# Optimization experiments

Measured on AMD Instinct MI355X. Metric: run time of the kernel, lower is better.

Reference implementation:

```python
import jax, jax.numpy as jnp
import numpy as np

NUM_AGENTS = 256
STATE_DIM = 12 * NUM_AGENTS
CONTROL_DIM = 4 * NUM_AGENTS
MASS = 0.5
HIDDEN = 100
BATCH = 8192


def lambertw(x):
    # Principal branch for x >= 0 via Halley iterations (jit/vjp friendly).
    w = jnp.log1p(x)
    for _ in range(30):
        ew = jnp.exp(w)
        f = w * ew - x
        denom = ew * (w + 1.0) - (w + 2.0) * f / (2.0 * (w + 1.0))
        w = w - f / denom
    return w


def setup_inputs() -> dict:
    key = jax.random.key(0)
    ks = jax.random.split(key, 8)
    scale1 = 1.0 / np.sqrt(STATE_DIM + 1)
    scale2 = 1.0 / np.sqrt(HIDDEN)
    return {
        "z": jax.random.normal(ks[0], (BATCH, STATE_DIM), dtype=jnp.float32),
        "t": jax.random.uniform(ks[1], (BATCH, 1), dtype=jnp.float32),
        "W1": jax.random.normal(ks[2], (STATE_DIM + 1, HIDDEN), dtype=jnp.float32) * scale1,
        "b1": jnp.zeros((HIDDEN,), dtype=jnp.float32),
        "W2": jax.random.normal(ks[3], (HIDDEN, HIDDEN), dtype=jnp.float32) * scale2,
        "b2": jnp.zeros((HIDDEN,), dtype=jnp.float32),
        "W3": jax.random.normal(ks[4], (HIDDEN, STATE_DIM), dtype=jnp.float32) * scale2,
        "b3": jnp.zeros((STATE_DIM,), dtype=jnp.float32),
    }


def reference(z, t, W1, b1, W2, b2, W3, b3):
    # p_net: MLP on (t, z) producing cost parameters p (B, STATE_DIM)
    x = jnp.concatenate([t, z], axis=-1)
    h = jnp.tanh(x @ W1 + b1)
    h = jnp.tanh(h @ W2 + b2)
    p = h @ W3 + b3

    B = p.shape[0]
    pr = p.reshape(B, NUM_AGENTS, 12)
    # Linear cost vector c over controls: agent components (x,y,z adjoints)/m, psi, theta, phi.
    c = jnp.stack(
        [(pr[..., 6] + pr[..., 7] + pr[..., 8]) / MASS, pr[..., 9], pr[..., 10], pr[..., 11]],
        axis=-1,
    ).reshape(B, CONTROL_DIM)

    # Closed-form solution of min_u c^T u + exp(alpha * ||u||^2), alpha = 0.5/N:
    # u* = -k c with 2*alpha*k*exp(alpha*k^2*s) = 1, s = ||c||^2
    # => k = sqrt(W(s/(2*alpha)) / (2*alpha*s))
    alpha = 0.5 / NUM_AGENTS
    s = jnp.sum(c * c, axis=-1)  # (B,)
    w = lambertw(s / (2.0 * alpha))
    safe_s = jnp.where(s > 0, s, 1.0)
    k = jnp.sqrt(w / (2.0 * alpha * safe_s))
    k = jnp.where(s > 0, k, 0.0)
    ustar = -k[:, None] * c  # (B, CONTROL_DIM)
    return ustar
```

## Files before the change

### kernel.cpp

```cpp
#include <hip/hip_runtime.h>

#define DEV __device__ __forceinline__

typedef __bf16 bf16x8 __attribute__((ext_vector_type(8)));
typedef float f32x4 __attribute__((ext_vector_type(4)));
typedef short s16x8 __attribute__((ext_vector_type(8)));
typedef unsigned short u16x4 __attribute__((ext_vector_type(4)));

constexpr int B_ = 8192;
constexpr int S_ = 3072;
constexpr int H_ = 100;
constexpr int NP_ = 128;
constexpr int C_ = 1024;
constexpr int KS_ = 64;
constexpr int NIT_ = S_ / KS_;

constexpr size_t OFF_W1b = 0;
constexpr size_t OFF_W2b = OFF_W1b + (size_t)NP_ * S_ * 2;
constexpr size_t OFF_W3c = OFF_W2b + (size_t)NP_ * NP_ * 2;
constexpr size_t OFF_b3c = OFF_W3c + (size_t)C_ * NP_ * 2;
constexpr size_t OFF_h2b = OFF_b3c + (size_t)C_ * 4;

DEV unsigned short f2bf(float f) {
  union { float f; unsigned u; } x; x.f = f;
  return (unsigned short)((x.u + 0x7FFFu + ((x.u >> 16) & 1u)) >> 16);
}

DEV float lambertw0(float x) {
  float w = log1pf(x);
#pragma unroll
  for (int i = 0; i < 10; ++i) {
    float ew = expf(w);
    float f = fmaf(w, ew, -x);
    float wp1 = w + 1.0f;
    float den = ew * wp1 - (w + 2.0f) * f / (2.0f * wp1);
    w = w - f / den;
  }
  return w;
}

__global__ void k0_prep(const float* __restrict__ W1, const float* __restrict__ W2,
                        const float* __restrict__ W3, const float* __restrict__ b3,
                        unsigned char* __restrict__ ws) {
  int idx = blockIdx.x * 256 + threadIdx.x;
  constexpr int R1 = NP_ * S_;
  constexpr int R2 = R1 + NP_ * NP_;
  constexpr int R3 = R2 + C_ * NP_;
  constexpr int R4 = R3 + C_;
  if (idx < R1) {
    int n = idx / S_, k = idx - n * S_;
    float v = (n < H_) ? W1[(size_t)(k + 1) * H_ + n] : 0.0f;
    ((unsigned short*)(ws + OFF_W1b))[idx] = f2bf(v);
  } else if (idx < R2) {
    int j = idx - R1;
    int n = j >> 7, k = j & 127;
    float v = (n < H_ && k < H_) ? W2[(size_t)k * H_ + n] : 0.0f;
    ((unsigned short*)(ws + OFF_W2b))[j] = f2bf(v);
  } else if (idx < R3) {
    int j = idx - R2;
    int n = j >> 7, k = j & 127;
    float v = 0.0f;
    if (k < H_) {
      int a = n >> 2, cmp = n & 3;
      const float* row = W3 + (size_t)k * S_ + a * 12;
      v = (cmp == 0) ? 2.0f * (row[6] + row[7] + row[8]) : row[8 + cmp];
    }
    ((unsigned short*)(ws + OFF_W3c))[j] = f2bf(v);
  } else if (idx < R4) {
    int n = idx - R3;
    int a = n >> 2, cmp = n & 3;
    const float* row = b3 + a * 12;
    float v = (cmp == 0) ? 2.0f * (row[6] + row[7] + row[8]) : row[8 + cmp];
    ((float*)(ws + OFF_b3c))[n] = v;
  }
}

__global__ __launch_bounds__(512, 2) void k1_mlp(
    const float* __restrict__ z, const float* __restrict__ t,
    const float* __restrict__ W1, const float* __restrict__ b1,
    const float* __restrict__ b2, const unsigned char* __restrict__ wsr,
    unsigned short* __restrict__ h2b) {
  __shared__ __align__(16) unsigned char lds[40 * 1024 + 128];
  unsigned char* ldsA = lds;
  unsigned char* ldsB = lds + 8192;
  float* t_lds = (float*)(lds + 40 * 1024);

  const int tid = threadIdx.x;
  const int lane = tid & 63;
  const int w = tid >> 6;
  const int m = w & 1;
  const int q = w >> 1;
  const int rowbase = blockIdx.x * 32;

  const unsigned short* W1b = (const unsigned short*)(wsr + OFF_W1b);
  const unsigned short* W2b = (const unsigned short*)(wsr + OFF_W2b);

  if (tid < 32) t_lds[tid] = t[rowbase + tid];

  float b1c[2], w1tc[2], b2c[2];
#pragma unroll
  for (int e = 0; e < 2; ++e) {
    int col = (q * 2 + e) * 16 + (lane & 15);
    bool ok = col < H_;
    b1c[e] = ok ? b1[col] : 0.0f;
    w1tc[e] = ok ? W1[col] : 0.0f;
    b2c[e] = ok ? b2[col] : 0.0f;
  }

  const int zrow = tid >> 4;
  const int zk4 = (tid & 15) * 4;
  const int r0 = m * 16 + (lane & 15);
  const int kb0 = (lane >> 4) * 16;

  f32x4 acc[2];
  acc[0] = f32x4{0.f, 0.f, 0.f, 0.f};
  acc[1] = f32x4{0.f, 0.f, 0.f, 0.f};

  {
    float4 zv = *(const float4*)(z + (size_t)(rowbase + zrow) * S_ + zk4);
    u16x4 av; av[0] = f2bf(zv.x); av[1] = f2bf(zv.y); av[2] = f2bf(zv.z); av[3] = f2bf(zv.w);
    *(u16x4*)(ldsA + ((zrow * 128 + zk4 * 2) ^ ((zrow & 7) << 4))) = av;
#pragma unroll
    for (int s = 0; s < 2; ++s) {
      int p = s * 512 + tid;
      int n = p >> 3, k16 = p & 7;
      s16x8 v = *(const s16x8*)(W1b + (size_t)n * S_ + k16 * 8);
      *(s16x8*)(ldsB + ((n * 128 + k16 * 16) ^ ((n & 7) << 4))) = v;
    }
  }
  __syncthreads();

  for (int it = 0; it < NIT_; ++it) {
    const int cur = it & 1;
    unsigned char* Ac = ldsA + cur * 4096;
    unsigned char* Bc = ldsB + cur * 16384;
    const bool more = (it + 1 < NIT_);
    float4 zv;
    s16x8 bv0, bv1;
    if (more) {
      int kb = (it + 1) * KS_;
      zv = *(const float4*)(z + (size_t)(rowbase + zrow) * S_ + kb + zk4);
      {
        int p = tid;          int n = p >> 3, k16 = p & 7;
        bv0 = *(const s16x8*)(W1b + (size_t)n * S_ + kb + k16 * 8);
      }
      {
        int p = 512 + tid;    int n = p >> 3, k16 = p & 7;
        bv1 = *(const s16x8*)(W1b + (size_t)n * S_ + kb + k16 * 8);
      }
    }
    bf16x8 a0 = *(const bf16x8*)(Ac + ((r0 * 128 + 0 + kb0) ^ ((r0 & 7) << 4)));
    bf16x8 a1 = *(const bf16x8*)(Ac + ((r0 * 128 + 64 + kb0) ^ ((r0 & 7) << 4)));
#pragma unroll
    for (int e = 0; e < 2; ++e) {
      int n = (q * 2 + e) * 16 + (lane & 15);
      bf16x8 bb0 = *(const bf16x8*)(Bc + ((n * 128 + 0 + kb0) ^ ((n & 7) << 4)));
      bf16x8 bb1 = *(const bf16x8*)(Bc + ((n * 128 + 64 + kb0) ^ ((n & 7) << 4)));
      acc[e] = __builtin_amdgcn_mfma_f32_16x16x32_bf16(a0, bb0, acc[e], 0, 0, 0);
      acc[e] = __builtin_amdgcn_mfma_f32_16x16x32_bf16(a1, bb1, acc[e], 0, 0, 0);
    }
    if (more) {
      unsigned char* An = ldsA + (cur ^ 1) * 4096;
      unsigned char* Bn = ldsB + (cur ^ 1) * 16384;
      u16x4 av; av[0] = f2bf(zv.x); av[1] = f2bf(zv.y); av[2] = f2bf(zv.z); av[3] = f2bf(zv.w);
      *(u16x4*)(An + ((zrow * 128 + zk4 * 2) ^ ((zrow & 7) << 4))) = av;
      {
        int p = tid;          int n = p >> 3, k16 = p & 7;
        *(s16x8*)(Bn + ((n * 128 + k16 * 16) ^ ((n & 7) << 4))) = bv0;
      }
      {
        int p = 512 + tid;    int n = p >> 3, k16 = p & 7;
        *(s16x8*)(Bn + ((n * 128 + k16 * 16) ^ ((n & 7) << 4))) = bv1;
      }
    }
    __syncthreads();
  }

#pragma unroll
  for (int e = 0; e < 2; ++e) {
    int col = (q * 2 + e) * 16 + (lane & 15);
#pragma unroll
    for (int i = 0; i < 4; ++i) {
      int r = m * 16 + ((lane >> 4) << 2) + i;
      float pre = acc[e][i] + b1c[e] + t_lds[r] * w1tc[e];
      *(unsigned short*)(ldsA + ((r * 256 + col * 2) ^ ((r & 7) << 4))) = f2bf(tanhf(pre));
    }
  }
#pragma unroll
  for (int s = 0; s < 4; ++s) {
    int p = s * 512 + tid;
    int n = p >> 4, k16 = p & 15;
    s16x8 v = *(const s16x8*)(W2b + n * 128 + k16 * 8);
    *(s16x8*)(ldsB + ((n * 256 + k16 * 16) ^ ((n & 7) << 4))) = v;
  }
  __syncthreads();

  f32x4 acc2[2];
  acc2[0] = f32x4{0.f, 0.f, 0.f, 0.f};
  acc2[1] = f32x4{0.f, 0.f, 0.f, 0.f};
#pragma unroll
  for (int ks = 0; ks < 4; ++ks) {
    bf16x8 a = *(const bf16x8*)(ldsA + ((r0 * 256 + ks * 64 + kb0) ^ ((r0 & 7) << 4)));
#pragma unroll
    for (int e = 0; e < 2; ++e) {
      int n = (q * 2 + e) * 16 + (lane & 15);
      bf16x8 b = *(const bf16x8*)(ldsB + ((n * 256 + ks * 64 + kb0) ^ ((n & 7) << 4)));
      acc2[e] = __builtin_amdgcn_mfma_f32_16x16x32_bf16(a, b, acc2[e], 0, 0, 0);
    }
  }
#pragma unroll
  for (int e = 0; e < 2; ++e) {
    int col = (q * 2 + e) * 16 + (lane & 15);
#pragma unroll
    for (int i = 0; i < 4; ++i) {
      int r = m * 16 + ((lane >> 4) << 2) + i;
      float h = tanhf(acc2[e][i] + b2c[e]);
      h2b[(size_t)(rowbase + r) * NP_ + col] = f2bf(h);
    }
  }
}

__global__ __launch_bounds__(512, 2) void k2_head(
    const unsigned char* __restrict__ wsr, float* __restrict__ uo) {
  __shared__ __align__(16) unsigned char ldsA[8192];
  __shared__ __align__(16) unsigned char ldsB[2][32768];
  __shared__ float s_part[32][4];
  __shared__ float k_lds[32];

  const int tid = threadIdx.x;
  const int lane = tid & 63;
  const int w = tid >> 6;
  const int m = w & 1;
  const int q = w >> 1;
  const int rowbase = blockIdx.x * 32;

  const unsigned short* h2b = (const unsigned short*)(wsr + OFF_h2b);
  const unsigned short* W3cb = (const unsigned short*)(wsr + OFF_W3c);
  const float* b3c = (const float*)(wsr + OFF_b3c);

  {
    int n = tid >> 4, k16 = tid & 15;
    s16x8 v = *(const s16x8*)(h2b + (size_t)(rowbase + n) * NP_ + k16 * 8);
    *(s16x8*)(ldsA + ((n * 256 + k16 * 16) ^ ((n & 7) << 4))) = v;
  }
#pragma unroll
  for (int s = 0; s < 4; ++s) {
    int p = s * 512 + tid;
    int n = p >> 4, k16 = p & 15;
    s16x8 v = *(const s16x8*)(W3cb + (size_t)n * NP_ + k16 * 8);
    *(s16x8*)(ldsB[0] + ((n * 256 + k16 * 16) ^ ((n & 7) << 4))) = v;
  }
  if (tid < 128) s_part[tid >> 2][tid & 3] = 0.0f;
  __syncthreads();

  const int r0 = m * 16 + (lane & 15);
  const int kb0 = (lane >> 4) * 16;
  bf16x8 af[4];
#pragma unroll
  for (int ks = 0; ks < 4; ++ks)
    af[ks] = *(const bf16x8*)(ldsA + ((r0 * 256 + ks * 64 + kb0) ^ ((r0 & 7) << 4)));

  f32x4 fr[16];
#pragma unroll
  for (int i = 0; i < 16; ++i) fr[i] = f32x4{0.f, 0.f, 0.f, 0.f};

#pragma unroll 8
  for (int ch = 0; ch < 8; ++ch) {
    const int cur = ch & 1;
    const bool more = ch < 7;
    s16x8 st0, st1, st2, st3;
    if (more) {
      int base = (ch + 1) * 128;
      { int p = tid;            int n = p >> 4, k16 = p & 15; st0 = *(const s16x8*)(W3cb + (size_t)(base + n) * NP_ + k16 * 8); }
      { int p = 512 + tid;      int n = p >> 4, k16 = p & 15; st1 = *(const s16x8*)(W3cb + (size_t)(base + n) * NP_ + k16 * 8); }
      { int p = 1024 + tid;     int n = p >> 4, k16 = p & 15; st2 = *(const s16x8*)(W3cb + (size_t)(base + n) * NP_ + k16 * 8); }
      { int p = 1536 + tid;     int n = p >> 4, k16 = p & 15; st3 = *(const s16x8*)(W3cb + (size_t)(base + n) * NP_ + k16 * 8); }
    }
#pragma unroll
    for (int e = 0; e < 2; ++e) {
      int nloc = (q + 4 * e) * 16 + (lane & 15);
#pragma unroll
      for (int ks = 0; ks < 4; ++ks) {
        bf16x8 b = *(const bf16x8*)(ldsB[cur] + ((nloc * 256 + ks * 64 + kb0) ^ ((nloc & 7) << 4)));
        fr[ch * 2 + e] = __builtin_amdgcn_mfma_f32_16x16x32_bf16(af[ks], b, fr[ch * 2 + e], 0, 0, 0);
      }
    }
    if (more) {
      unsigned char* Bn = ldsB[cur ^ 1];
      { int p = tid;        int n = p >> 4, k16 = p & 15; *(s16x8*)(Bn + ((n * 256 + k16 * 16) ^ ((n & 7) << 4))) = st0; }
      { int p = 512 + tid;  int n = p >> 4, k16 = p & 15; *(s16x8*)(Bn + ((n * 256 + k16 * 16) ^ ((n & 7) << 4))) = st1; }
      { int p = 1024 + tid; int n = p >> 4, k16 = p & 15; *(s16x8*)(Bn + ((n * 256 + k16 * 16) ^ ((n & 7) << 4))) = st2; }
      { int p = 1536 + tid; int n = p >> 4, k16 = p & 15; *(s16x8*)(Bn + ((n * 256 + k16 * 16) ^ ((n & 7) << 4))) = st3; }
    }
    __syncthreads();
  }

#pragma unroll
  for (int fi = 0; fi < 16; ++fi) {
    int ch = fi >> 1, e = fi & 1;
    int col = (ch * 8 + q + 4 * e) * 16 + (lane & 15);
    float bc = b3c[col];
    fr[fi][0] += bc; fr[fi][1] += bc; fr[fi][2] += bc; fr[fi][3] += bc;
  }
#pragma unroll
  for (int i = 0; i < 4; ++i) {
    float v = 0.f;
#pragma unroll
    for (int fi = 0; fi < 16; ++fi) v += fr[fi][i] * fr[fi][i];
    v += __shfl_xor(v, 1);
    v += __shfl_xor(v, 2);
    v += __shfl_xor(v, 4);
    v += __shfl_xor(v, 8);
    if ((lane & 15) == 0) s_part[m * 16 + ((lane >> 4) << 2) + i][q] = v;
  }
  __syncthreads();
  if (tid < 32) {
    float s = s_part[tid][0] + s_part[tid][1] + s_part[tid][2] + s_part[tid][3];
    float kk = 0.0f;
    if (s > 0.0f) {
      float wv = lambertw0(s * 256.0f);
      kk = sqrtf(wv * 256.0f / s);
    }
    k_lds[tid] = kk;
  }
  __syncthreads();
#pragma unroll
  for (int fi = 0; fi < 16; ++fi) {
    int ch = fi >> 1, e = fi & 1;
    int col = (ch * 8 + q + 4 * e) * 16 + (lane & 15);
#pragma unroll
    for (int i = 0; i < 4; ++i) {
      int r = m * 16 + ((lane >> 4) << 2) + i;
      uo[(size_t)(rowbase + r) * C_ + col] = -k_lds[r] * fr[fi][i];
    }
  }
}

extern "C" void kernel_launch(void* const* d_in, const int* in_sizes, int n_in,
                              void* d_out, int out_size, void* d_ws, size_t ws_size,
                              hipStream_t stream) {
  const float* z  = (const float*)d_in[0];
  const float* t  = (const float*)d_in[1];
  const float* W1 = (const float*)d_in[2];
  const float* b1 = (const float*)d_in[3];
  const float* W2 = (const float*)d_in[4];
  const float* b2 = (const float*)d_in[5];
  const float* W3 = (const float*)d_in[6];
  const float* b3 = (const float*)d_in[7];
  float* out = (float*)d_out;
  unsigned char* ws = (unsigned char*)d_ws;

  constexpr int PREP_ELEMS = NP_ * S_ + NP_ * NP_ + C_ * NP_ + C_;
  k0_prep<<<(PREP_ELEMS + 255) / 256, 256, 0, stream>>>(W1, W2, W3, b3, ws);
  k1_mlp<<<B_ / 32, 512, 0, stream>>>(z, t, W1, b1, b2, ws,
                                      (unsigned short*)(ws + OFF_h2b));
  k2_head<<<B_ / 32, 512, 0, stream>>>(ws, out);
}
```

Before: 59.10 us.

## Split first GEMM over K into four blocks with partial-sum reduction kernel

The first layer GEMM (B×3072 by 3072×128) is split along K into four independent blocks per row tile, each writing fp32 partial sums into the output buffer used as scratch. A new kernel sums the partials, applies bias, time term and tanh, then runs layer two. Block size drops to 256 threads with four waves each covering 64 columns. This raises grid parallelism from 256 to 1024 blocks to fill the GPU's compute units better, at the cost of an extra 16 MB partial write/read and an added kernel launch.

```diff
diff --git a/kernel.cpp b/kernel.cpp
--- a/kernel.cpp
+++ b/kernel.cpp
@@ -6,6 +6,7 @@
 typedef float f32x4 __attribute__((ext_vector_type(4)));
 typedef short s16x8 __attribute__((ext_vector_type(8)));
 typedef unsigned short u16x4 __attribute__((ext_vector_type(4)));
+typedef unsigned short u16x8 __attribute__((ext_vector_type(8)));
 
 constexpr int B_ = 8192;
 constexpr int S_ = 3072;
@@ -13,7 +14,9 @@
 constexpr int NP_ = 128;
 constexpr int C_ = 1024;
 constexpr int KS_ = 64;
-constexpr int NIT_ = S_ / KS_;
+constexpr int NSPLIT_ = 4;
+constexpr int KSP_ = S_ / NSPLIT_;
+constexpr int NIT_ = KSP_ / KS_;
 
 constexpr size_t OFF_W1b = 0;
 constexpr size_t OFF_W2b = OFF_W1b + (size_t)NP_ * S_ * 2;
@@ -75,15 +78,120 @@
   }
 }
 
-__global__ __launch_bounds__(512, 2) void k1_mlp(
-    const float* __restrict__ z, const float* __restrict__ t,
+__global__ __launch_bounds__(256, 4) void k1_gemm1(
+    const float* __restrict__ z, const unsigned char* __restrict__ wsr,
+    float* __restrict__ part) {
+  __shared__ __align__(16) unsigned char lds[40 * 1024];
+  unsigned char* ldsA = lds;
+  unsigned char* ldsB = lds + 8192;
+
+  const int tid = threadIdx.x;
+  const int lane = tid & 63;
+  const int w = tid >> 6;
+  const int m = w & 1;
+  const int q = w >> 1;
+  const int bid = blockIdx.x;
+  const int rt = bid >> 2;
+  const int h = bid & 3;
+  const int rowbase = rt * 32;
+  const int k0 = h * KSP_;
+
+  const unsigned short* W1b = (const unsigned short*)(wsr + OFF_W1b);
+
+  const int zrow = tid >> 3;
+  const int zk8 = (tid & 7) * 8;
+  const float* zp = z + (size_t)(rowbase + zrow) * S_ + k0 + zk8;
+  const int bn = tid >> 3;
+  const int bk16 = (tid & 7) * 8;
+  const unsigned short* bp = W1b + (size_t)bn * S_ + k0 + bk16;
+
+  const int aswz = ((zrow & 7) << 4);
+  const int abyte = zrow * 128 + zk8 * 2;
+  const int bswz = ((bn & 7) << 4);
+  const int bbyte0 = bn * 128 + bk16 * 2;
+
+  const int r0 = m * 16 + (lane & 15);
+  const int kb0 = (lane >> 4) * 16;
+
+  f32x4 acc[4];
+#pragma unroll
+  for (int e = 0; e < 4; ++e) acc[e] = f32x4{0.f, 0.f, 0.f, 0.f};
+
+  {
+    float4 za = *(const float4*)(zp);
+    float4 zb = *(const float4*)(zp + 4);
+    u16x8 av;
+    av[0] = f2bf(za.x); av[1] = f2bf(za.y); av[2] = f2bf(za.z); av[3] = f2bf(za.w);
+    av[4] = f2bf(zb.x); av[5] = f2bf(zb.y); av[6] = f2bf(zb.z); av[7] = f2bf(zb.w);
+    *(u16x8*)(ldsA + (abyte ^ aswz)) = av;
+#pragma unroll
+    for (int s = 0; s < 4; ++s) {
+      s16x8 v = *(const s16x8*)(bp + (size_t)(s * 32) * S_);
+      *(s16x8*)(ldsB + ((bbyte0 + s * 32 * 128) ^ bswz)) = v;
+    }
+  }
+  __syncthreads();
+
+  for (int it = 0; it < NIT_; ++it) {
+    const int cur = it & 1;
+    unsigned char* Ac = ldsA + cur * 4096;
+    unsigned char* Bc = ldsB + cur * 16384;
+    const bool more = (it + 1 < NIT_);
+    float4 za, zb;
+    s16x8 bv0, bv1, bv2, bv3;
+    if (more) {
+      const int ko = (it + 1) * KS_;
+      za = *(const float4*)(zp + ko);
+      zb = *(const float4*)(zp + ko + 4);
+      bv0 = *(const s16x8*)(bp + ko);
+      bv1 = *(const s16x8*)(bp + ko + (size_t)32 * S_);
+      bv2 = *(const s16x8*)(bp + ko + (size_t)64 * S_);
+      bv3 = *(const s16x8*)(bp + ko + (size_t)96 * S_);
+    }
+    bf16x8 a0 = *(const bf16x8*)(Ac + ((r0 * 128 + 0 + kb0) ^ ((r0 & 7) << 4)));
+    bf16x8 a1 = *(const bf16x8*)(Ac + ((r0 * 128 + 64 + kb0) ^ ((r0 & 7) << 4)));
+#pragma unroll
+    for (int e = 0; e < 4; ++e) {
+      int n = q * 64 + e * 16 + (lane & 15);
+      bf16x8 bb0 = *(const bf16x8*)(Bc + ((n * 128 + 0 + kb0) ^ ((n & 7) << 4)));
+      bf16x8 bb1 = *(const bf16x8*)(Bc + ((n * 128 + 64 + kb0) ^ ((n & 7) << 4)));
+      acc[e] = __builtin_amdgcn_mfma_f32_16x16x32_bf16(a0, bb0, acc[e], 0, 0, 0);
+      acc[e] = __builtin_amdgcn_mfma_f32_16x16x32_bf16(a1, bb1, acc[e], 0, 0, 0);
+    }
+    if (more) {
+      unsigned char* An = ldsA + (cur ^ 1) * 4096;
+      unsigned char* Bn = ldsB + (cur ^ 1) * 16384;
+      u16x8 av;
+      av[0] = f2bf(za.x); av[1] = f2bf(za.y); av[2] = f2bf(za.z); av[3] = f2bf(za.w);
+      av[4] = f2bf(zb.x); av[5] = f2bf(zb.y); av[6] = f2bf(zb.z); av[7] = f2bf(zb.w);
+      *(u16x8*)(An + (abyte ^ aswz)) = av;
+      *(s16x8*)(Bn + ((bbyte0 + 0 * 32 * 128) ^ bswz)) = bv0;
+      *(s16x8*)(Bn + ((bbyte0 + 1 * 32 * 128) ^ bswz)) = bv1;
+      *(s16x8*)(Bn + ((bbyte0 + 2 * 32 * 128) ^ bswz)) = bv2;
+      *(s16x8*)(Bn + ((bbyte0 + 3 * 32 * 128) ^ bswz)) = bv3;
+    }
+    __syncthreads();
+  }
+
+  float* pout = part + (size_t)h * B_ * NP_;
+#pragma unroll
+  for (int e = 0; e < 4; ++e) {
+    int col = q * 64 + e * 16 + (lane & 15);
+#pragma unroll
+    for (int i = 0; i < 4; ++i) {
+      int r = m * 16 + ((lane >> 4) << 2) + i;
+      pout[(size_t)(rowbase + r) * NP_ + col] = acc[e][i];
+    }
+  }
+}
+
+__global__ __launch_bounds__(256, 4) void k2a_mlp(
+    const float* __restrict__ part, const float* __restrict__ t,
     const float* __restrict__ W1, const float* __restrict__ b1,
     const float* __restrict__ b2, const unsigned char* __restrict__ wsr,
     unsigned short* __restrict__ h2b) {
-  __shared__ __align__(16) unsigned char lds[40 * 1024 + 128];
-  unsigned char* ldsA = lds;
-  unsigned char* ldsB = lds + 8192;
-  float* t_lds = (float*)(lds + 40 * 1024);
+  __shared__ __align__(16) unsigned char ldsA[8192];
+  __shared__ __align__(16) unsigned char ldsB[32768];
 
   const int tid = threadIdx.x;
   const int lane = tid & 63;
@@ -92,130 +200,70 @@
   const int q = w >> 1;
   const int rowbase = blockIdx.x * 32;
 
-  const unsigned short* W1b = (const unsigned short*)(wsr + OFF_W1b);
   const unsigned short* W2b = (const unsigned short*)(wsr + OFF_W2b);
 
-  if (tid < 32) t_lds[tid] = t[rowbase + tid];
-
-  float b1c[2], w1tc[2], b2c[2];
-#pragma unroll
-  for (int e = 0; e < 2; ++e) {
-    int col = (q * 2 + e) * 16 + (lane & 15);
-    bool ok = col < H_;
-    b1c[e] = ok ? b1[col] : 0.0f;
-    w1tc[e] = ok ? W1[col] : 0.0f;
-    b2c[e] = ok ? b2[col] : 0.0f;
-  }
-
-  const int zrow = tid >> 4;
-  const int zk4 = (tid & 15) * 4;
-  const int r0 = m * 16 + (lane & 15);
-  const int kb0 = (lane >> 4) * 16;
-
-  f32x4 acc[2];
-  acc[0] = f32x4{0.f, 0.f, 0.f, 0.f};
-  acc[1] = f32x4{0.f, 0.f, 0.f, 0.f};
-
   {
-    float4 zv = *(const float4*)(z + (size_t)(rowbase + zrow) * S_ + zk4);
-    u16x4 av; av[0] = f2bf(zv.x); av[1] = f2bf(zv.y); av[2] = f2bf(zv.z); av[3] = f2bf(zv.w);
-    *(u16x4*)(ldsA + ((zrow * 128 + zk4 * 2) ^ ((zrow & 7) << 4))) = av;
-#pragma unroll
-    for (int s = 0; s < 2; ++s) {
-      int p = s * 512 + tid;
-      int n = p >> 3, k16 = p & 7;
-      s16x8 v = *(const s16x8*)(W1b + (size_t)n * S_ + k16 * 8);
-      *(s16x8*)(ldsB + ((n * 128 + k16 * 16) ^ ((n & 7) << 4))) = v;
-    }
-  }
-  __syncthreads();
-
-  for (int it = 0; it < NIT_; ++it) {
-    const int cur = it & 1;
-    unsigned char* Ac = ldsA + cur * 4096;
-    unsigned char* Bc = ldsB + cur * 16384;
-    const bool more = (it + 1 < NIT_);
-    float4 zv;
-    s16x8 bv0, bv1;
-    if (more) {
-      int kb = (it + 1) * KS_;
-      zv = *(const float4*)(z + (size_t)(rowbase + zrow) * S_ + kb + zk4);
-      {
-        int p = tid;          int n = p >> 3, k16 = p & 7;
-        bv0 = *(const s16x8*)(W1b + (size_t)n * S_ + kb + k16 * 8);
+    const int row = tid >> 3;
+    const int col0 = (tid & 7) * 16;
+    const float* p0 = part + (size_t)(rowbase + row) * NP_ + col0;
+    f32x4 v[4];
+#pragma unroll
+    for (int p = 0; p < 4; ++p) {
+      v[p] = *(const f32x4*)(p0 + p * 4);
+#pragma unroll
+      for (int hh = 1; hh < NSPLIT_; ++hh) {
+        f32x4 u = *(const f32x4*)(p0 + (size_t)hh * B_ * NP_ + p * 4);
+        v[p][0] += u[0]; v[p][1] += u[1]; v[p][2] += u[2]; v[p][3] += u[3];
       }
-      {
-        int p = 512 + tid;    int n = p >> 3, k16 = p & 7;
-        bv1 = *(const s16x8*)(W1b + (size_t)n * S_ + kb + k16 * 8);
-      }
-    }
-    bf16x8 a0 = *(const bf16x8*)(Ac + ((r0 * 128 + 0 + kb0) ^ ((r0 & 7) << 4)));
-    bf16x8 a1 = *(const bf16x8*)(Ac + ((r0 * 128 + 64 + kb0) ^ ((r0 & 7) << 4)));
-#pragma unroll
-    for (int e = 0; e < 2; ++e) {
-      int n = (q * 2 + e) * 16 + (lane & 15);
-      bf16x8 bb0 = *(const bf16x8*)(Bc + ((n * 128 + 0 + kb0) ^ ((n & 7) << 4)));
-      bf16x8 bb1 = *(const bf16x8*)(Bc + ((n * 128 + 64 + kb0) ^ ((n & 7) << 4)));
-      acc[e] = __builtin_amdgcn_mfma_f32_16x16x32_bf16(a0, bb0, acc[e], 0, 0, 0);
-      acc[e] = __builtin_amdgcn_mfma_f32_16x16x32_bf16(a1, bb1, acc[e], 0, 0, 0);
-    }
-    if (more) {
-      unsigned char* An = ldsA + (cur ^ 1) * 4096;
-      unsigned char* Bn = ldsB + (cur ^ 1) * 16384;
-      u16x4 av; av[0] = f2bf(zv.x); av[1] = f2bf(zv.y); av[2] = f2bf(zv.z); av[3] = f2bf(zv.w);
-      *(u16x4*)(An + ((zrow * 128 + zk4 * 2) ^ ((zrow & 7) << 4))) = av;
-      {
-        int p = tid;          int n = p >> 3, k16 = p & 7;
-        *(s16x8*)(Bn + ((n * 128 + k16 * 16) ^ ((n & 7) << 4))) = bv0;
-      }
-      {
-        int p = 512 + tid;    int n = p >> 3, k16 = p & 7;
-        *(s16x8*)(Bn + ((n * 128 + k16 * 16) ^ ((n & 7) << 4))) = bv1;
-      }
-    }
-    __syncthreads();
-  }
-
-#pragma unroll
-  for (int e = 0; e < 2; ++e) {
-    int col = (q * 2 + e) * 16 + (lane & 15);
-#pragma unroll
-    for (int i = 0; i < 4; ++i) {
-      int r = m * 16 + ((lane >> 4) << 2) + i;
-      float pre = acc[e][i] + b1c[e] + t_lds[r] * w1tc[e];
-      *(unsigned short*)(ldsA + ((r * 256 + col * 2) ^ ((r & 7) << 4))) = f2bf(tanhf(pre));
-    }
-  }
-#pragma unroll
-  for (int s = 0; s < 4; ++s) {
-    int p = s * 512 + tid;
+    }
+    const float tv = t[rowbase + row];
+    u16x8 o0, o1;
+#pragma unroll
+    for (int j = 0; j < 16; ++j) {
+      int col = col0 + j;
+      float b1c = (col < H_) ? b1[col] : 0.0f;
+      float w1t = (col < H_) ? W1[col] : 0.0f;
+      float pre = v[j >> 2][j & 3] + b1c + tv * w1t;
+      unsigned short hb = f2bf(tanhf(pre));
+      if (j < 8) o0[j] = hb; else o1[j - 8] = hb;
+    }
+    const int sw = ((row & 7) << 4);
+    *(u16x8*)(ldsA + ((row * 256 + col0 * 2) ^ sw)) = o0;
+    *(u16x8*)(ldsA + ((row * 256 + (col0 + 8) * 2) ^ sw)) = o1;
+  }
+#pragma unroll
+  for (int s = 0; s < 8; ++s) {
+    int p = s * 256 + tid;
     int n = p >> 4, k16 = p & 15;
     s16x8 v = *(const s16x8*)(W2b + n * 128 + k16 * 8);
     *(s16x8*)(ldsB + ((n * 256 + k16 * 16) ^ ((n & 7) << 4))) = v;
   }
   __syncthreads();
 
-  f32x4 acc2[2];
-  acc2[0] = f32x4{0.f, 0.f, 0.f, 0.f};
-  acc2[1] = f32x4{0.f, 0.f, 0.f, 0.f};
+  const int r0 = m * 16 + (lane & 15);
+  const int kb0 = (lane >> 4) * 16;
+  f32x4 acc[4];
+#pragma unroll
+  for (int e = 0; e < 4; ++e) acc[e] = f32x4{0.f, 0.f, 0.f, 0.f};
 #pragma unroll
   for (int ks = 0; ks < 4; ++ks) {
     bf16x8 a = *(const bf16x8*)(ldsA + ((r0 * 256 + ks * 64 + kb0) ^ ((r0 & 7) << 4)));
 #pragma unroll
-    for (int e = 0; e < 2; ++e) {
-      int n = (q * 2 + e) * 16 + (lane & 15);
+    for (int e = 0; e < 4; ++e) {
+      int n = q * 64 + e * 16 + (lane & 15);
       bf16x8 b = *(const bf16x8*)(ldsB + ((n * 256 + ks * 64 + kb0) ^ ((n & 7) << 4)));
-      acc2[e] = __builtin_amdgcn_mfma_f32_16x16x32_bf16(a, b, acc2[e], 0, 0, 0);
-    }
-  }
-#pragma unroll
-  for (int e = 0; e < 2; ++e) {
-    int col = (q * 2 + e) * 16 + (lane & 15);
+      acc[e] = __builtin_amdgcn_mfma_f32_16x16x32_bf16(a, b, acc[e], 0, 0, 0);
+    }
+  }
+#pragma unroll
+  for (int e = 0; e < 4; ++e) {
+    int col = q * 64 + e * 16 + (lane & 15);
+    float b2c = (col < H_) ? b2[col] : 0.0f;
 #pragma unroll
     for (int i = 0; i < 4; ++i) {
       int r = m * 16 + ((lane >> 4) << 2) + i;
-      float h = tanhf(acc2[e][i] + b2c[e]);
-      h2b[(size_t)(rowbase + r) * NP_ + col] = f2bf(h);
+      float hh = tanhf(acc[e][i] + b2c);
+      h2b[(size_t)(rowbase + r) * NP_ + col] = f2bf(hh);
     }
   }
 }
@@ -352,7 +400,8 @@
 
   constexpr int PREP_ELEMS = NP_ * S_ + NP_ * NP_ + C_ * NP_ + C_;
   k0_prep<<<(PREP_ELEMS + 255) / 256, 256, 0, stream>>>(W1, W2, W3, b3, ws);
-  k1_mlp<<<B_ / 32, 512, 0, stream>>>(z, t, W1, b1, b2, ws,
-                                      (unsigned short*)(ws + OFF_h2b));
+  k1_gemm1<<<B_ / 32 * NSPLIT_, 256, 0, stream>>>(z, ws, out);
+  k2a_mlp<<<B_ / 32, 256, 0, stream>>>(out, t, W1, b1, b2, ws,
+                                       (unsigned short*)(ws + OFF_h2b));
   k2_head<<<B_ / 32, 512, 0, stream>>>(ws, out);
 }
```

Result: faster. 57.49 us (-2.7%).
